# Performance work log

Measured on AMD Instinct MI355X. Metric: run time of the kernel, lower is better.

Reference implementation:

```python
import jax, jax.numpy as jnp
import numpy as np

ITEM_SIZE = 100000
USER_SIZE = 1000000
K = 64
B = 1048576


def setup_inputs() -> dict:
    key = jax.random.key(0)
    k1, k2, k3, k4, k5, k6 = jax.random.split(key, 6)
    u = jax.random.randint(k1, (B,), 0, USER_SIZE, dtype=jnp.int64 if jax.config.read('jax_enable_x64') else jnp.int32)
    i = jax.random.randint(k2, (B,), 0, ITEM_SIZE, dtype=u.dtype)
    s = jax.random.randint(k3, (B,), 0, 2, dtype=u.dtype)
    # xavier_normal-style init (gain=1): std = sqrt(2/(fan_in+fan_out))
    diff = jax.random.normal(k4, (ITEM_SIZE, 1), dtype=jnp.float32) * np.sqrt(2.0 / (ITEM_SIZE + 1))
    disc = jax.random.normal(k5, (ITEM_SIZE, K), dtype=jnp.float32) * np.sqrt(2.0 / (ITEM_SIZE + K))
    theta = jax.random.normal(k6, (USER_SIZE, K), dtype=jnp.float32) * np.sqrt(2.0 / (USER_SIZE + K))
    return {"u": u, "i": i, "s": s, "diff": diff, "disc": disc, "theta": theta}


def reference(u, i, s, diff, disc, theta):
    # Original computes eye(B) * (disc[i] @ theta[u].T) then sums rows:
    # that is exactly the per-pair dot product, computed here directly.
    disc_i = disc[i]            # [B, k] gather
    theta_u = theta[u]          # [B, k] gather
    x = jnp.sum(disc_i * theta_u, axis=1, keepdims=True) + diff[i]  # [B, 1]
    real = s.astype(jnp.float32)[:, None]                            # [B, 1]
    # BCE(sigmoid(x), real), numerically stable via log_sigmoid
    loss = -jnp.mean(real * jax.nn.log_sigmoid(x) + (1.0 - real) * jax.nn.log_sigmoid(-x))
    return loss
```

## Files before the change

kernel.cpp:

```cpp
#include <hip/hip_runtime.h>


__global__ void zero_out_kernel(float* out) { out[0] = 0.0f; }

__global__ __launch_bounds__(256) void mirt_loss_kernel(
    const int* __restrict__ u,
    const int* __restrict__ iidx,
    const int* __restrict__ s,
    const float* __restrict__ diff,
    const float* __restrict__ disc,
    const float* __restrict__ theta,
    float* __restrict__ out,
    int B, float inv_b)
{
    const int lane16 = threadIdx.x & 15;
    const int groupInBlock = threadIdx.x >> 4;
    const int groupsPerBlock = blockDim.x >> 4;
    const int stride = gridDim.x * groupsPerBlock;
    int pair = blockIdx.x * groupsPerBlock + groupInBlock;

    float acc = 0.0f;
    for (; pair < B; pair += stride) {
        const int uu = u[pair];
        const int ii = iidx[pair];
        const float4 t4 = ((const float4*)(theta + (size_t)uu * 64))[lane16];
        const float4 d4 = ((const float4*)(disc  + (size_t)ii * 64))[lane16];
        float p = t4.x * d4.x + t4.y * d4.y + t4.z * d4.z + t4.w * d4.w;
        p += __shfl_xor(p, 1);
        p += __shfl_xor(p, 2);
        p += __shfl_xor(p, 4);
        p += __shfl_xor(p, 8);
        if (lane16 == 0) {
            const float x = p + diff[ii];
            const float z = (s[pair] != 0) ? -x : x;
            acc += fmaxf(z, 0.0f) + log1pf(__expf(-fabsf(z)));
        }
    }

    acc += __shfl_xor(acc, 32);
    acc += __shfl_xor(acc, 16);
    acc += __shfl_xor(acc, 8);
    acc += __shfl_xor(acc, 4);
    acc += __shfl_xor(acc, 2);
    acc += __shfl_xor(acc, 1);

    __shared__ float wave_sums[4];
    const int wave = threadIdx.x >> 6;
    const int lane = threadIdx.x & 63;
    if (lane == 0) wave_sums[wave] = acc;
    __syncthreads();
    if (threadIdx.x == 0) {
        const float bs = wave_sums[0] + wave_sums[1] + wave_sums[2] + wave_sums[3];
        atomicAdd(out, bs * inv_b);
    }
}

extern "C" void kernel_launch(void* const* d_in, const int* in_sizes, int n_in,
                              void* d_out, int out_size, void* d_ws, size_t ws_size,
                              hipStream_t stream) {
    const int*   u     = (const int*)d_in[0];
    const int*   iidx  = (const int*)d_in[1];
    const int*   s     = (const int*)d_in[2];
    const float* diff  = (const float*)d_in[3];
    const float* disc  = (const float*)d_in[4];
    const float* theta = (const float*)d_in[5];
    float* out = (float*)d_out;

    const int B = in_sizes[0];

    zero_out_kernel<<<1, 1, 0, stream>>>(out);

    const int block = 256;
    const int grid = 4096;
    mirt_loss_kernel<<<grid, block, 0, stream>>>(
        u, iidx, s, diff, disc, theta, out, B, 1.0f / (float)B);
}
```

Baseline: 411.1 us.

## Prefetch next pair indices and replace atomic accumulation with two-pass reduction

The loop now loads the u, i and s indices for the next iteration before issuing the dependent gathers for the current pair, so index load latency overlaps with the row gathers. The diff load is hoisted so every lane issues it with the vector loads. The zero-out kernel and per-block atomicAdd are replaced by per-block partials written to workspace and a single-block final reduction kernel. This costs a few extra registers and keeps a second small launch, but gives deterministic summation and removes atomic contention.

```diff
diff --git a/kernel.cpp b/kernel.cpp
--- a/kernel.cpp
+++ b/kernel.cpp
@@ -1,17 +1,17 @@
 #include <hip/hip_runtime.h>
 
 
-__global__ void zero_out_kernel(float* out) { out[0] = 0.0f; }
+#define GRID_BLOCKS 4096
 
-__global__ __launch_bounds__(256) void mirt_loss_kernel(
+__global__ __launch_bounds__(256) void mirt_partial_kernel(
     const int* __restrict__ u,
     const int* __restrict__ iidx,
     const int* __restrict__ s,
     const float* __restrict__ diff,
     const float* __restrict__ disc,
     const float* __restrict__ theta,
-    float* __restrict__ out,
-    int B, float inv_b)
+    float* __restrict__ partials,
+    int B)
 {
     const int lane16 = threadIdx.x & 15;
     const int groupInBlock = threadIdx.x >> 4;
@@ -19,22 +19,32 @@
     const int stride = gridDim.x * groupsPerBlock;
     int pair = blockIdx.x * groupsPerBlock + groupInBlock;
 
+    int uu = 0, ii = 0, ss = 0;
+    if (pair < B) { uu = u[pair]; ii = iidx[pair]; ss = s[pair]; }
+
     float acc = 0.0f;
-    for (; pair < B; pair += stride) {
-        const int uu = u[pair];
-        const int ii = iidx[pair];
+    for (; pair < B; ) {
+        const int npair = pair + stride;
+        int nuu = 0, nii = 0, nss = 0;
+        if (npair < B) {
+            nuu = u[npair];
+            nii = iidx[npair];
+            nss = s[npair];
+        }
         const float4 t4 = ((const float4*)(theta + (size_t)uu * 64))[lane16];
         const float4 d4 = ((const float4*)(disc  + (size_t)ii * 64))[lane16];
+        const float df  = diff[ii];
         float p = t4.x * d4.x + t4.y * d4.y + t4.z * d4.z + t4.w * d4.w;
         p += __shfl_xor(p, 1);
         p += __shfl_xor(p, 2);
         p += __shfl_xor(p, 4);
         p += __shfl_xor(p, 8);
         if (lane16 == 0) {
-            const float x = p + diff[ii];
-            const float z = (s[pair] != 0) ? -x : x;
+            const float x = p + df;
+            const float z = (ss != 0) ? -x : x;
             acc += fmaxf(z, 0.0f) + log1pf(__expf(-fabsf(z)));
         }
+        pair = npair; uu = nuu; ii = nii; ss = nss;
     }
 
     acc += __shfl_xor(acc, 32);
@@ -50,8 +60,33 @@
     if (lane == 0) wave_sums[wave] = acc;
     __syncthreads();
     if (threadIdx.x == 0) {
-        const float bs = wave_sums[0] + wave_sums[1] + wave_sums[2] + wave_sums[3];
-        atomicAdd(out, bs * inv_b);
+        partials[blockIdx.x] =
+            wave_sums[0] + wave_sums[1] + wave_sums[2] + wave_sums[3];
+    }
+}
+
+__global__ __launch_bounds__(256) void mirt_final_kernel(
+    const float* __restrict__ partials, float* __restrict__ out,
+    int n, float inv_b)
+{
+    float acc = 0.0f;
+    for (int j = threadIdx.x; j < n; j += 256) acc += partials[j];
+
+    acc += __shfl_xor(acc, 32);
+    acc += __shfl_xor(acc, 16);
+    acc += __shfl_xor(acc, 8);
+    acc += __shfl_xor(acc, 4);
+    acc += __shfl_xor(acc, 2);
+    acc += __shfl_xor(acc, 1);
+
+    __shared__ float wave_sums[4];
+    const int wave = threadIdx.x >> 6;
+    const int lane = threadIdx.x & 63;
+    if (lane == 0) wave_sums[wave] = acc;
+    __syncthreads();
+    if (threadIdx.x == 0) {
+        out[0] = (wave_sums[0] + wave_sums[1] + wave_sums[2] + wave_sums[3])
+                 * inv_b;
     }
 }
 
@@ -64,14 +99,13 @@
     const float* diff  = (const float*)d_in[3];
     const float* disc  = (const float*)d_in[4];
     const float* theta = (const float*)d_in[5];
-    float* out = (float*)d_out;
+    float* out      = (float*)d_out;
+    float* partials = (float*)d_ws;
 
     const int B = in_sizes[0];
 
-    zero_out_kernel<<<1, 1, 0, stream>>>(out);
-
-    const int block = 256;
-    const int grid = 4096;
-    mirt_loss_kernel<<<grid, block, 0, stream>>>(
-        u, iidx, s, diff, disc, theta, out, B, 1.0f / (float)B);
+    mirt_partial_kernel<<<GRID_BLOCKS, 256, 0, stream>>>(
+        u, iidx, s, diff, disc, theta, partials, B);
+    mirt_final_kernel<<<1, 256, 0, stream>>>(
+        partials, out, GRID_BLOCKS, 1.0f / (float)B);
 }
```

New measurement: 392.0 us. 4.6% less time.
